# Performance work log

Measured on AMD Instinct MI355X. Metric: run time of the kernel, lower is better.

The kernel has to match this reference:

```python
import jax, jax.numpy as jnp
import numpy as np

BIG = 1e9
EPS_BETA = 1e-6
EPS_BN = 1e-5

N_NODES = 50000
N_EDGES = 800000
IN_DIM = 128
OUT_DIM = 128


def setup_inputs() -> dict:
    key = jax.random.key(0)
    ks = jax.random.split(key, 8)
    h = jax.random.normal(ks[0], (N_NODES, IN_DIM), dtype=jnp.float32)
    src = jax.random.randint(ks[1], (N_EDGES,), 0, N_NODES, dtype=jnp.int32)
    dst = jax.random.randint(ks[2], (N_EDGES,), 0, N_NODES, dtype=jnp.int32)
    sigma_GD = jax.random.uniform(ks[3], (N_EDGES,), dtype=jnp.float32)
    fc_w = jax.random.normal(ks[4], (IN_DIM, OUT_DIM), dtype=jnp.float32) / np.sqrt(IN_DIM)
    fc_b = jax.random.normal(ks[5], (OUT_DIM,), dtype=jnp.float32) * 0.01
    attn_w = jax.random.normal(ks[6], (2 * OUT_DIM, 1), dtype=jnp.float32) / np.sqrt(2 * OUT_DIM)
    attn_b = jax.random.normal(ks[7], (1,), dtype=jnp.float32) * 0.01
    bn_gamma = jnp.ones((OUT_DIM,), dtype=jnp.float32)
    bn_beta = jnp.zeros((OUT_DIM,), dtype=jnp.float32)
    return {"h": h, "src": src, "dst": dst, "sigma_GD": sigma_GD,
            "fc_w": fc_w, "fc_b": fc_b, "attn_w": attn_w, "attn_b": attn_b,
            "bn_gamma": bn_gamma, "bn_beta": bn_beta}


def reference(h, src, dst, sigma_GD, fc_w, fc_b, attn_w, attn_b, bn_gamma, bn_beta):
    n = h.shape[0]
    # node projection
    z = h @ fc_w + fc_b                                   # [N, D]
    z = jnp.where(jnp.isinf(z), BIG, z)
    # per-edge attention logits: concat(src,dst) @ W == src@W1 + dst@W2 (avoid concat materialization)
    d = z.shape[1]
    w_src, w_dst = attn_w[:d], attn_w[d:]
    z_src = z[src]                                        # [E, D]
    a = z_src @ w_src + z[dst] @ w_dst + attn_b           # [E, 1]
    a = jnp.where(jnp.isinf(a), BIG, a)
    e = jax.nn.leaky_relu(a, negative_slope=0.01)[:, 0]   # [E]
    # segment softmax over incoming edges (mailbox softmax)
    m = jax.ops.segment_max(e, dst, num_segments=n)       # [N]
    ex = jnp.exp(e - m[dst])
    denom = jax.ops.segment_sum(ex, dst, num_segments=n)  # [N]
    alpha = ex / denom[dst]                               # [E]
    # beta: sigma_GD normalized per destination node
    bsum = jax.ops.segment_sum(sigma_GD, dst, num_segments=n)
    beta = sigma_GD / (bsum[dst] + EPS_BETA)              # [E]
    # weighted scatter-sum of source features
    h_new = jax.ops.segment_sum((alpha * beta)[:, None] * z_src, dst, num_segments=n)  # [N, D]
    h_new = jnp.where(jnp.isinf(h_new), BIG, h_new)
    # BatchNorm1d (training-mode batch stats, biased variance, as torch does)
    mu = h_new.mean(axis=0)
    var = ((h_new - mu) ** 2).mean(axis=0)
    h_bn = (h_new - mu) * jax.lax.rsqrt(var + EPS_BN) * bn_gamma + bn_beta
    return jax.nn.elu(h_bn)
```

## Files before the change

kernel.cpp:

```cpp
#include <hip/hip_runtime.h>
#include <hip/hip_fp16.h>
#include <math.h>

#define N_NODES 50000
#define N_EDGES 800000
#define BIGV 1000000000.0f
#define NBLK_GEMM 3125
#define CHUNK 1024
#define NCHUNK 782
#define NBUCKET 782
#define NB4 784

typedef _Float16 half8 __attribute__((ext_vector_type(8)));
typedef float floatx4 __attribute__((ext_vector_type(4)));

__device__ __forceinline__ float clampinf(float x) { return isinf(x) ? BIGV : x; }

__device__ __forceinline__ void barrier_lgkm_only() {
    __builtin_amdgcn_sched_barrier(0);
    asm volatile("s_waitcnt lgkmcnt(0)" ::: "memory");
    __builtin_amdgcn_s_barrier();
    __builtin_amdgcn_sched_barrier(0);
}

__global__ __launch_bounds__(256) void k_prep(const float* __restrict__ W,
                                              __half* __restrict__ wt,
                                              float* __restrict__ bns,
                                              const int* __restrict__ dst,
                                              int* __restrict__ countsT)
{
    __shared__ int hist[NB4];
    const int t = threadIdx.x;
    const int idx = blockIdx.x * 256 + t;
    if (idx < 16384) {
        int n = idx >> 7, k = idx & 127;
        wt[idx] = __float2half(W[k * 128 + n]);
    }
    if (idx < 256) bns[idx] = 0.f;
    for (int i = t; i < NB4; i += 256) hist[i] = 0;
    __syncthreads();
    const int base = blockIdx.x * CHUNK;
    for (int i = t; i < CHUNK; i += 256) {
        int e = base + i;
        if (e < N_EDGES) atomicAdd(&hist[dst[e] >> 6], 1);
    }
    __syncthreads();
    for (int i = t; i < NB4; i += 256)
        countsT[i * NB4 + blockIdx.x] = hist[i];
}

__global__ __launch_bounds__(256) void k_off(const int* __restrict__ countsT,
                                             int* __restrict__ cursC,
                                             int* __restrict__ btot)
{
    const int wv = (blockIdx.x << 2) + (threadIdx.x >> 6);
    const int l = threadIdx.x & 63;
    if (wv >= NBUCKET) {
        if (l == 0 && wv < NB4) btot[wv] = 0;
        return;
    }
    const int* row = countsT + (size_t)wv * NB4;
    int carry = 0;
    #pragma unroll
    for (int p = 0; p < 13; ++p) {
        const int c = p * 64 + l;
        const int v = (c < NCHUNK) ? row[c] : 0;
        int x = v;
        #pragma unroll
        for (int o = 1; o < 64; o <<= 1) {
            int u = __shfl_up(x, o);
            if (l >= o) x += u;
        }
        if (c < NCHUNK) cursC[(size_t)c * NB4 + wv] = carry + x - v;
        carry += __shfl(x, 63);
    }
    if (l == 0) btot[wv] = carry;
}

__global__ __launch_bounds__(256) void k_gemm(
    const float* __restrict__ h, const __half* __restrict__ wt,
    const float* __restrict__ bias, const float* __restrict__ attn_w,
    __half* __restrict__ zh, float* __restrict__ sv, float* __restrict__ tv)
{
    __shared__ _Float16 hA[16][136];
    __shared__ float spart[4][16], tpart[4][16];

    const int tid = threadIdx.x;
    const int lane = tid & 63;
    const int wv = tid >> 6;
    const int l16 = lane & 15;
    const int oct = lane >> 4;
    const int n0 = wv << 5;
    const int node0 = blockIdx.x << 4;

    {
        const float4* h4 = (const float4*)(h + (size_t)node0 * 128);
        for (int i = tid; i < 512; i += 256) {
            int r = i >> 5, c4 = i & 31;
            float4 v = h4[i];
            union { __half2 h2[2]; uint2 u; } pk;
            pk.h2[0] = __floats2half2_rn(v.x, v.y);
            pk.h2[1] = __floats2half2_rn(v.z, v.w);
            *(uint2*)&hA[r][c4 << 2] = pk.u;
        }
    }

    half8 bfrag[4][2];
    #pragma unroll
    for (int kk = 0; kk < 4; ++kk)
        #pragma unroll
        for (int t = 0; t < 2; ++t)
            bfrag[kk][t] = *(const half8*)(wt + (size_t)(n0 + t * 16 + l16) * 128
                                              + kk * 32 + oct * 8);

    const float bv0 = bias[n0 + l16],         bv1 = bias[n0 + 16 + l16];
    const float ws0 = attn_w[n0 + l16],       ws1 = attn_w[n0 + 16 + l16];
    const float wd0 = attn_w[128 + n0 + l16], wd1 = attn_w[128 + n0 + 16 + l16];

    barrier_lgkm_only();

    floatx4 acc0 = {0.f, 0.f, 0.f, 0.f};
    floatx4 acc1 = {0.f, 0.f, 0.f, 0.f};
    #pragma unroll
    for (int kk = 0; kk < 4; ++kk) {
        half8 a = *(const half8*)&hA[l16][(kk << 5) + (oct << 3)];
        acc0 = __builtin_amdgcn_mfma_f32_16x16x32_f16(a, bfrag[kk][0], acc0, 0, 0, 0);
        acc1 = __builtin_amdgcn_mfma_f32_16x16x32_f16(a, bfrag[kk][1], acc1, 0, 0, 0);
    }

    float s_acc[4], t_acc[4];
    #pragma unroll
    for (int r = 0; r < 4; ++r) {
        float z0 = clampinf(acc0[r] + bv0);
        float z1 = clampinf(acc1[r] + bv1);
        const int row = (oct << 2) + r;
        zh[(size_t)(node0 + row) * 128 + n0 + l16]      = __float2half(z0);
        zh[(size_t)(node0 + row) * 128 + n0 + 16 + l16] = __float2half(z1);
        s_acc[r] = z0 * ws0 + z1 * ws1;
        t_acc[r] = z0 * wd0 + z1 * wd1;
    }
    #pragma unroll
    for (int r = 0; r < 4; ++r) {
        #pragma unroll
        for (int o = 1; o < 16; o <<= 1) {
            s_acc[r] += __shfl_xor(s_acc[r], o);
            t_acc[r] += __shfl_xor(t_acc[r], o);
        }
    }
    if (l16 == 0) {
        #pragma unroll
        for (int r = 0; r < 4; ++r) {
            spart[wv][(oct << 2) + r] = s_acc[r];
            tpart[wv][(oct << 2) + r] = t_acc[r];
        }
    }
    barrier_lgkm_only();
    if (tid < 16) {
        sv[node0 + tid] = spart[0][tid] + spart[1][tid] + spart[2][tid] + spart[3][tid];
        tv[node0 + tid] = tpart[0][tid] + tpart[1][tid] + tpart[2][tid] + tpart[3][tid];
    }
}

__global__ __launch_bounds__(256) void k_scat(
    const int* __restrict__ src, const int* __restrict__ dst,
    const float* __restrict__ sigma,
    const float* __restrict__ sv, const float* __restrict__ tv,
    const float* __restrict__ attn_b,
    const int* __restrict__ cursC, const int* __restrict__ btot,
    float4* __restrict__ tmp, int* __restrict__ bbase_g)
{
    __shared__ int cur[NB4];
    __shared__ int bb[NB4];
    __shared__ int tsc[256];
    const int t = threadIdx.x;
    const int self = blockIdx.x;

    for (int i = t; i < NB4; i += 256) cur[i] = cursC[(size_t)self * NB4 + i];

    uint4 bt = {0u, 0u, 0u, 0u};
    int tsum = 0;
    if (t < 196) {
        bt = ((const uint4*)btot)[t];
        tsum = (int)(bt.x + bt.y + bt.z + bt.w);
    }
    tsc[t] = tsum;
    __syncthreads();
    for (int off = 1; off < 256; off <<= 1) {
        int u = (t >= off) ? tsc[t - off] : 0;
        __syncthreads();
        tsc[t] += u;
        __syncthreads();
    }
    if (t < 196) {
        const int v0 = tsc[t] - tsum;
        bb[4*t+0] = v0;
        bb[4*t+1] = v0 + (int)bt.x;
        bb[4*t+2] = v0 + (int)bt.x + (int)bt.y;
        bb[4*t+3] = v0 + (int)bt.x + (int)bt.y + (int)bt.z;
    }
    __syncthreads();
    for (int i = t; i < NB4; i += 256) cur[i] += bb[i];
    if (self == 0)
        for (int i = t; i < NB4; i += 256) bbase_g[i] = bb[i];
    __syncthreads();

    const float ab = attn_b[0];
    const int base = self * CHUNK;
    for (int i = t; i < CHUNK; i += 256) {
        int e = base + i;
        if (e < N_EDGES) {
            int s = src[e];
            int d = dst[e];
            float a = sv[s] + tv[d] + ab;
            a = clampinf(a);
            float ev = a > 0.f ? a : 0.01f * a;
            int pos = atomicAdd(&cur[d >> 6], 1);
            float4 rec;
            rec.x = __int_as_float(s);
            rec.y = sigma[e];
            rec.z = ev;
            rec.w = __int_as_float(d);
            tmp[pos] = rec;
        }
    }
}

__global__ __launch_bounds__(256) void k_binB(const float4* __restrict__ tmp,
                                              const int* __restrict__ bbase_g,
                                              int* __restrict__ colptr,
                                              float4* __restrict__ recs)
{
    __shared__ int hist[64];
    __shared__ int cur[64];
    const int t = threadIdx.x;
    const int b = blockIdx.x;
    const int s0 = bbase_g[b];
    const int n = ((b + 1 < NB4) ? bbase_g[b + 1] : N_EDGES) - s0;
    if (t < 64) hist[t] = 0;
    __syncthreads();
    const float* tw = (const float*)tmp;
    for (int i = t; i < n; i += 256) {
        int d = __float_as_int(tw[4 * (size_t)(s0 + i) + 3]);
        atomicAdd(&hist[d & 63], 1);
    }
    __syncthreads();
    if (t < 64) {
        const int hv = hist[t];
        int x = hv;
        #pragma unroll
        for (int o = 1; o < 64; o <<= 1) {
            int u = __shfl_up(x, o);
            if (t >= o) x += u;
        }
        const int excl = x - hv;
        cur[t] = s0 + excl;
        const int node = (b << 6) + t;
        if (node < N_NODES) colptr[node] = s0 + excl;
    }
    if (b == 0 && t == 0) colptr[N_NODES] = N_EDGES;
    __syncthreads();
    for (int i = t; i < n; i += 256) {
        float4 rec = tmp[s0 + i];
        int d = __float_as_int(rec.w);
        int pos = atomicAdd(&cur[d & 63], 1);
        rec.w = 0.f;
        recs[pos] = rec;
    }
}

__global__ __launch_bounds__(256) void k_agg(
    const int* __restrict__ colptr, const float4* __restrict__ recs,
    const __half* __restrict__ zh, float* __restrict__ out)
{
    const int lane = threadIdx.x & 63;
    const int node = blockIdx.x * 4 + (threadIdx.x >> 6);
    if (node >= N_NODES) return;
    const int base = colptr[node];
    const int deg = colptr[node + 1] - base;

    const int grp = lane >> 4;
    const int l16 = lane & 15;
    float acc[8] = {0.f, 0.f, 0.f, 0.f, 0.f, 0.f, 0.f, 0.f};

    if (deg > 0) {
        if (deg <= 64) {
            int sidx = 0; float sig = 0.f, e = -INFINITY;
            if (lane < deg) {
                float4 r = recs[base + lane];
                sidx = __float_as_int(r.x); sig = r.y; e = r.z;
            }
            float m = e;
            for (int o = 32; o; o >>= 1) m = fmaxf(m, __shfl_xor(m, o));
            float p = (lane < deg) ? __expf(e - m) : 0.f;
            float dn = p, bs = sig;
            for (int o = 32; o; o >>= 1) {
                dn += __shfl_xor(dn, o);
                bs += __shfl_xor(bs, o);
            }
            const float coef = p * sig * (1.0f / dn) / (bs + 1e-6f);
            for (int c = 0; c < deg; c += 4) {
                const int j = c + grp;
                const int js = (j < deg) ? j : 0;
                float cf = __shfl(coef, js);
                int sj = __shfl(sidx, js);
                if (j < deg) {
                    uint4 raw = *(const uint4*)(zh + ((size_t)sj << 7) + (l16 << 3));
                    const __half2* hp = (const __half2*)&raw;
                    #pragma unroll
                    for (int k = 0; k < 4; ++k) {
                        float2 f = __half22float2(hp[k]);
                        acc[2*k]   = fmaf(cf, f.x, acc[2*k]);
                        acc[2*k+1] = fmaf(cf, f.y, acc[2*k+1]);
                    }
                }
            }
        } else {
            float m = -INFINITY;
            for (int i = lane; i < deg; i += 64) m = fmaxf(m, recs[base + i].z);
            for (int o = 32; o; o >>= 1) m = fmaxf(m, __shfl_xor(m, o));
            float dn = 0.f, bs = 0.f;
            for (int i = lane; i < deg; i += 64) {
                float4 r = recs[base + i];
                dn += __expf(r.z - m); bs += r.y;
            }
            for (int o = 32; o; o >>= 1) {
                dn += __shfl_xor(dn, o);
                bs += __shfl_xor(bs, o);
            }
            const float scale = (1.0f / dn) / (bs + 1e-6f);
            for (int c = 0; c < deg; c += 64) {
                int i = c + lane;
                int sidx = 0; float coef = 0.f;
                if (i < deg) {
                    float4 r = recs[base + i];
                    sidx = __float_as_int(r.x);
                    coef = __expf(r.z - m) * r.y * scale;
                }
                const int cnt2 = min(64, deg - c);
                for (int j = 0; j < cnt2; j += 4) {
                    const int jj = j + grp;
                    const int js = (jj < cnt2) ? jj : 0;
                    float cf = __shfl(coef, js);
                    int sj = __shfl(sidx, js);
                    if (jj < cnt2) {
                        uint4 raw = *(const uint4*)(zh + ((size_t)sj << 7) + (l16 << 3));
                        const __half2* hp = (const __half2*)&raw;
                        #pragma unroll
                        for (int k = 0; k < 4; ++k) {
                            float2 f = __half22float2(hp[k]);
                            acc[2*k]   = fmaf(cf, f.x, acc[2*k]);
                            acc[2*k+1] = fmaf(cf, f.y, acc[2*k+1]);
                        }
                    }
                }
            }
        }
    }
    #pragma unroll
    for (int k = 0; k < 8; ++k) {
        acc[k] += __shfl_xor(acc[k], 16);
        acc[k] += __shfl_xor(acc[k], 32);
    }
    if (grp == 0) {
        float4 o0, o1;
        o0.x = clampinf(acc[0]); o0.y = clampinf(acc[1]);
        o0.z = clampinf(acc[2]); o0.w = clampinf(acc[3]);
        o1.x = clampinf(acc[4]); o1.y = clampinf(acc[5]);
        o1.z = clampinf(acc[6]); o1.w = clampinf(acc[7]);
        float4* op = (float4*)(out + (size_t)node * 128 + (l16 << 3));
        op[0] = o0; op[1] = o1;
    }
}

__global__ __launch_bounds__(256) void k_bnstats(const float* __restrict__ hnew,
                                                 float* __restrict__ sums)
{
    const int tid = threadIdx.x;
    const int f4 = (tid & 31) << 2;
    const int rgrp = tid >> 5;
    float4 s = {0.f, 0.f, 0.f, 0.f}, q = {0.f, 0.f, 0.f, 0.f};
    for (int node = blockIdx.x * 8 + rgrp; node < N_NODES; node += 256 * 8) {
        float4 v = *(const float4*)(hnew + (size_t)node * 128 + f4);
        s.x += v.x; s.y += v.y; s.z += v.z; s.w += v.w;
        q.x += v.x * v.x; q.y += v.y * v.y; q.z += v.z * v.z; q.w += v.w * v.w;
    }
    __shared__ float4 ls[256], lq[256];
    ls[tid] = s; lq[tid] = q;
    __syncthreads();
    for (int off = 128; off >= 32; off >>= 1) {
        if (tid < off) {
            float4 a = ls[tid + off], b = lq[tid + off];
            ls[tid].x += a.x; ls[tid].y += a.y; ls[tid].z += a.z; ls[tid].w += a.w;
            lq[tid].x += b.x; lq[tid].y += b.y; lq[tid].z += b.z; lq[tid].w += b.w;
        }
        __syncthreads();
    }
    if (tid < 32) {
        float4 fs = ls[tid], fq = lq[tid];
        atomicAdd(&sums[f4 + 0], fs.x);
        atomicAdd(&sums[f4 + 1], fs.y);
        atomicAdd(&sums[f4 + 2], fs.z);
        atomicAdd(&sums[f4 + 3], fs.w);
        atomicAdd(&sums[128 + f4 + 0], fq.x);
        atomicAdd(&sums[128 + f4 + 1], fq.y);
        atomicAdd(&sums[128 + f4 + 2], fq.z);
        atomicAdd(&sums[128 + f4 + 3], fq.w);
    }
}

__global__ __launch_bounds__(256) void k_bnapply(float* __restrict__ io,
                                                 const float* __restrict__ sums,
                                                 const float* __restrict__ gamma,
                                                 const float* __restrict__ beta)
{
    __shared__ float sc[128], sh[128];
    const int tid = threadIdx.x;
    if (tid < 128) {
        const float invn = 1.0f / (float)N_NODES;
        float mu = sums[tid] * invn;
        float var = fmaxf(sums[128 + tid] * invn - mu * mu, 0.f);
        float g = gamma[tid] * rsqrtf(var + 1e-5f);
        sc[tid] = g;
        sh[tid] = beta[tid] - mu * g;
    }
    __syncthreads();
    const size_t idx = (size_t)blockIdx.x * 256 + tid;
    const int f4 = ((int)idx & 31) << 2;
    float4 x = ((const float4*)io)[idx];
    float y0 = x.x * sc[f4 + 0] + sh[f4 + 0];
    float y1 = x.y * sc[f4 + 1] + sh[f4 + 1];
    float y2 = x.z * sc[f4 + 2] + sh[f4 + 2];
    float y3 = x.w * sc[f4 + 3] + sh[f4 + 3];
    float4 o;
    o.x = y0 > 0.f ? y0 : expm1f(y0);
    o.y = y1 > 0.f ? y1 : expm1f(y1);
    o.z = y2 > 0.f ? y2 : expm1f(y2);
    o.w = y3 > 0.f ? y3 : expm1f(y3);
    ((float4*)io)[idx] = o;
}

extern "C" void kernel_launch(void* const* d_in, const int* in_sizes, int n_in,
                              void* d_out, int out_size, void* d_ws, size_t ws_size,
                              hipStream_t stream)
{
    const float* h      = (const float*)d_in[0];
    const int*   src    = (const int*)  d_in[1];
    const int*   dst    = (const int*)  d_in[2];
    const float* sigma  = (const float*)d_in[3];
    const float* fc_w   = (const float*)d_in[4];
    const float* fc_b   = (const float*)d_in[5];
    const float* attn_w = (const float*)d_in[6];
    const float* attn_b = (const float*)d_in[7];
    const float* gamma  = (const float*)d_in[8];
    const float* beta   = (const float*)d_in[9];
    float* out = (float*)d_out;

    float4* recs   = (float4*)d_ws;
    float4* tmp    = recs + N_EDGES;
    __half* zh     = (__half*)(tmp + N_EDGES);
    float*  sv     = (float*)(zh + (size_t)N_NODES * 128);
    float*  tv     = sv + N_NODES;
    float*  bns    = tv + N_NODES;
    int*    colptr = (int*)(bns + 256);
    __half* wt     = (__half*)(colptr + 50004);
    int*    countsT= (int*)(wt + 16384);
    int*    cursC  = countsT + NB4 * NB4;
    int*    btot   = cursC + NB4 * NB4;
    int*    bbase  = btot + NB4;

    k_prep    <<<NCHUNK, 256, 0, stream>>>(fc_w, wt, bns, dst, countsT);
    k_off     <<<196, 256, 0, stream>>>(countsT, cursC, btot);
    k_gemm    <<<NBLK_GEMM, 256, 0, stream>>>(h, wt, fc_b, attn_w, zh, sv, tv);
    k_scat    <<<NCHUNK, 256, 0, stream>>>(src, dst, sigma, sv, tv, attn_b,
                                           cursC, btot, tmp, bbase);
    k_binB    <<<NBUCKET, 256, 0, stream>>>(tmp, bbase, colptr, recs);
    k_agg     <<<N_NODES / 4, 256, 0, stream>>>(colptr, recs, zh, out);
    k_bnstats <<<256, 256, 0, stream>>>(out, bns);
    k_bnapply <<<(N_NODES * 128) / (256 * 4), 256, 0, stream>>>(out, bns, gamma, beta);
}
```

Baseline: 225.4 us.

## Fuse second-level binning with aggregation in LDS; deterministic BN partial reduction

The per-bucket local sort and the per-node aggregation are merged into one kernel. Each bucket's edge records are sorted into shared memory, with a global overflow buffer for buckets larger than the LDS capacity, and each of 8 waves then aggregates its nodes straight from LDS. This removes the global recs/colptr write and reread and one kernel launch, at the cost of fewer, larger blocks (782 blocks of 512 threads) for the gather-heavy aggregation. BN statistics now write per-block partials that a single-block kernel reduces, replacing float atomics and the zero-init.

```diff
diff --git a/kernel.cpp b/kernel.cpp
--- a/kernel.cpp
+++ b/kernel.cpp
@@ -10,6 +10,8 @@
 #define NCHUNK 782
 #define NBUCKET 782
 #define NB4 784
+#define BMAX 1280
+#define NBLK_BN 512
 
 typedef _Float16 half8 __attribute__((ext_vector_type(8)));
 typedef float floatx4 __attribute__((ext_vector_type(4)));
@@ -25,7 +27,6 @@
 
 __global__ __launch_bounds__(256) void k_prep(const float* __restrict__ W,
                                               __half* __restrict__ wt,
-                                              float* __restrict__ bns,
                                               const int* __restrict__ dst,
                                               int* __restrict__ countsT)
 {
@@ -36,7 +37,6 @@
         int n = idx >> 7, k = idx & 127;
         wt[idx] = __float2half(W[k * 128 + n]);
     }
-    if (idx < 256) bns[idx] = 0.f;
     for (int i = t; i < NB4; i += 256) hist[i] = 0;
     __syncthreads();
     const int base = blockIdx.x * CHUNK;
@@ -225,21 +225,24 @@
     }
 }
 
-__global__ __launch_bounds__(256) void k_binB(const float4* __restrict__ tmp,
-                                              const int* __restrict__ bbase_g,
-                                              int* __restrict__ colptr,
-                                              float4* __restrict__ recs)
-{
+__global__ __launch_bounds__(512) void k_bagg(
+    const float4* __restrict__ tmp, const int* __restrict__ bbase_g,
+    const __half* __restrict__ zh, float4* __restrict__ ovf,
+    float* __restrict__ out)
+{
+    __shared__ float4 lrec[BMAX];
     __shared__ int hist[64];
+    __shared__ int segs[65];
     __shared__ int cur[64];
     const int t = threadIdx.x;
     const int b = blockIdx.x;
     const int s0 = bbase_g[b];
-    const int n = ((b + 1 < NB4) ? bbase_g[b + 1] : N_EDGES) - s0;
+    const int n = bbase_g[b + 1] - s0;
+
     if (t < 64) hist[t] = 0;
     __syncthreads();
     const float* tw = (const float*)tmp;
-    for (int i = t; i < n; i += 256) {
+    for (int i = t; i < n; i += 512) {
         int d = __float_as_int(tw[4 * (size_t)(s0 + i) + 3]);
         atomicAdd(&hist[d & 63], 1);
     }
@@ -252,97 +255,55 @@
             int u = __shfl_up(x, o);
             if (t >= o) x += u;
         }
-        const int excl = x - hv;
-        cur[t] = s0 + excl;
-        const int node = (b << 6) + t;
-        if (node < N_NODES) colptr[node] = s0 + excl;
-    }
-    if (b == 0 && t == 0) colptr[N_NODES] = N_EDGES;
-    __syncthreads();
-    for (int i = t; i < n; i += 256) {
+        segs[t] = x - hv;
+        cur[t]  = x - hv;
+        if (t == 63) segs[64] = x;
+    }
+    __syncthreads();
+    for (int i = t; i < n; i += 512) {
         float4 rec = tmp[s0 + i];
         int d = __float_as_int(rec.w);
         int pos = atomicAdd(&cur[d & 63], 1);
-        rec.w = 0.f;
-        recs[pos] = rec;
-    }
-}
-
-__global__ __launch_bounds__(256) void k_agg(
-    const int* __restrict__ colptr, const float4* __restrict__ recs,
-    const __half* __restrict__ zh, float* __restrict__ out)
-{
-    const int lane = threadIdx.x & 63;
-    const int node = blockIdx.x * 4 + (threadIdx.x >> 6);
-    if (node >= N_NODES) return;
-    const int base = colptr[node];
-    const int deg = colptr[node + 1] - base;
-
+        if (pos < BMAX) lrec[pos] = rec;
+        else            ovf[s0 + pos] = rec;
+    }
+    __syncthreads();
+
+    const int lane = t & 63;
+    const int wv = t >> 6;
     const int grp = lane >> 4;
     const int l16 = lane & 15;
-    float acc[8] = {0.f, 0.f, 0.f, 0.f, 0.f, 0.f, 0.f, 0.f};
-
-    if (deg > 0) {
-        if (deg <= 64) {
-            int sidx = 0; float sig = 0.f, e = -INFINITY;
-            if (lane < deg) {
-                float4 r = recs[base + lane];
-                sidx = __float_as_int(r.x); sig = r.y; e = r.z;
-            }
-            float m = e;
-            for (int o = 32; o; o >>= 1) m = fmaxf(m, __shfl_xor(m, o));
-            float p = (lane < deg) ? __expf(e - m) : 0.f;
-            float dn = p, bs = sig;
-            for (int o = 32; o; o >>= 1) {
-                dn += __shfl_xor(dn, o);
-                bs += __shfl_xor(bs, o);
-            }
-            const float coef = p * sig * (1.0f / dn) / (bs + 1e-6f);
-            for (int c = 0; c < deg; c += 4) {
-                const int j = c + grp;
-                const int js = (j < deg) ? j : 0;
-                float cf = __shfl(coef, js);
-                int sj = __shfl(sidx, js);
-                if (j < deg) {
-                    uint4 raw = *(const uint4*)(zh + ((size_t)sj << 7) + (l16 << 3));
-                    const __half2* hp = (const __half2*)&raw;
-                    #pragma unroll
-                    for (int k = 0; k < 4; ++k) {
-                        float2 f = __half22float2(hp[k]);
-                        acc[2*k]   = fmaf(cf, f.x, acc[2*k]);
-                        acc[2*k+1] = fmaf(cf, f.y, acc[2*k+1]);
-                    }
-                }
-            }
-        } else {
-            float m = -INFINITY;
-            for (int i = lane; i < deg; i += 64) m = fmaxf(m, recs[base + i].z);
-            for (int o = 32; o; o >>= 1) m = fmaxf(m, __shfl_xor(m, o));
-            float dn = 0.f, bs = 0.f;
-            for (int i = lane; i < deg; i += 64) {
-                float4 r = recs[base + i];
-                dn += __expf(r.z - m); bs += r.y;
-            }
-            for (int o = 32; o; o >>= 1) {
-                dn += __shfl_xor(dn, o);
-                bs += __shfl_xor(bs, o);
-            }
-            const float scale = (1.0f / dn) / (bs + 1e-6f);
-            for (int c = 0; c < deg; c += 64) {
-                int i = c + lane;
-                int sidx = 0; float coef = 0.f;
-                if (i < deg) {
-                    float4 r = recs[base + i];
-                    sidx = __float_as_int(r.x);
-                    coef = __expf(r.z - m) * r.y * scale;
-                }
-                const int cnt2 = min(64, deg - c);
-                for (int j = 0; j < cnt2; j += 4) {
-                    const int jj = j + grp;
-                    const int js = (jj < cnt2) ? jj : 0;
+
+    for (int j = wv; j < 64; j += 8) {
+        const int node = (b << 6) + j;
+        if (node >= N_NODES) continue;
+        const int beg = segs[j];
+        const int deg = segs[j + 1] - beg;
+        float acc[8] = {0.f, 0.f, 0.f, 0.f, 0.f, 0.f, 0.f, 0.f};
+
+        if (deg > 0) {
+            if (deg <= 64) {
+                int sidx = 0; float sig = 0.f, e = -INFINITY;
+                if (lane < deg) {
+                    const int off = beg + lane;
+                    float4 r = (off < BMAX) ? lrec[off] : ovf[s0 + off];
+                    sidx = __float_as_int(r.x); sig = r.y; e = r.z;
+                }
+                float m = e;
+                for (int o = 32; o; o >>= 1) m = fmaxf(m, __shfl_xor(m, o));
+                float p = (lane < deg) ? __expf(e - m) : 0.f;
+                float dn = p, bs = sig;
+                for (int o = 32; o; o >>= 1) {
+                    dn += __shfl_xor(dn, o);
+                    bs += __shfl_xor(bs, o);
+                }
+                const float coef = p * sig * (1.0f / dn) / (bs + 1e-6f);
+                for (int c = 0; c < deg; c += 4) {
+                    const int jj = c + grp;
+                    const int js = (jj < deg) ? jj : 0;
                     float cf = __shfl(coef, js);
                     int sj = __shfl(sidx, js);
-                    if (jj < cnt2) {
+                    if (jj < deg) {
                         uint4 raw = *(const uint4*)(zh + ((size_t)sj << 7) + (l16 << 3));
                         const __half2* hp = (const __half2*)&raw;
                         #pragma unroll
@@ -353,33 +314,79 @@
                         }
                     }
                 }
+            } else {
+                float m = -INFINITY;
+                for (int i = lane; i < deg; i += 64) {
+                    const int off = beg + i;
+                    float4 r = (off < BMAX) ? lrec[off] : ovf[s0 + off];
+                    m = fmaxf(m, r.z);
+                }
+                for (int o = 32; o; o >>= 1) m = fmaxf(m, __shfl_xor(m, o));
+                float dn = 0.f, bs = 0.f;
+                for (int i = lane; i < deg; i += 64) {
+                    const int off = beg + i;
+                    float4 r = (off < BMAX) ? lrec[off] : ovf[s0 + off];
+                    dn += __expf(r.z - m); bs += r.y;
+                }
+                for (int o = 32; o; o >>= 1) {
+                    dn += __shfl_xor(dn, o);
+                    bs += __shfl_xor(bs, o);
+                }
+                const float scale = (1.0f / dn) / (bs + 1e-6f);
+                for (int c = 0; c < deg; c += 64) {
+                    int i = c + lane;
+                    int sidx = 0; float coef = 0.f;
+                    if (i < deg) {
+                        const int off = beg + i;
+                        float4 r = (off < BMAX) ? lrec[off] : ovf[s0 + off];
+                        sidx = __float_as_int(r.x);
+                        coef = __expf(r.z - m) * r.y * scale;
+                    }
+                    const int cnt2 = min(64, deg - c);
+                    for (int jj = 0; jj < cnt2; jj += 4) {
+                        const int j4 = jj + grp;
+                        const int js = (j4 < cnt2) ? j4 : 0;
+                        float cf = __shfl(coef, js);
+                        int sj = __shfl(sidx, js);
+                        if (j4 < cnt2) {
+                            uint4 raw = *(const uint4*)(zh + ((size_t)sj << 7) + (l16 << 3));
+                            const __half2* hp = (const __half2*)&raw;
+                            #pragma unroll
+                            for (int k = 0; k < 4; ++k) {
+                                float2 f = __half22float2(hp[k]);
+                                acc[2*k]   = fmaf(cf, f.x, acc[2*k]);
+                                acc[2*k+1] = fmaf(cf, f.y, acc[2*k+1]);
+                            }
+                        }
+                    }
+                }
             }
         }
-    }
-    #pragma unroll
-    for (int k = 0; k < 8; ++k) {
-        acc[k] += __shfl_xor(acc[k], 16);
-        acc[k] += __shfl_xor(acc[k], 32);
-    }
-    if (grp == 0) {
-        float4 o0, o1;
-        o0.x = clampinf(acc[0]); o0.y = clampinf(acc[1]);
-        o0.z = clampinf(acc[2]); o0.w = clampinf(acc[3]);
-        o1.x = clampinf(acc[4]); o1.y = clampinf(acc[5]);
-        o1.z = clampinf(acc[6]); o1.w = clampinf(acc[7]);
-        float4* op = (float4*)(out + (size_t)node * 128 + (l16 << 3));
-        op[0] = o0; op[1] = o1;
+        #pragma unroll
+        for (int k = 0; k < 8; ++k) {
+            acc[k] += __shfl_xor(acc[k], 16);
+            acc[k] += __shfl_xor(acc[k], 32);
+        }
+        if (grp == 0) {
+            float4 o0, o1;
+            o0.x = clampinf(acc[0]); o0.y = clampinf(acc[1]);
+            o0.z = clampinf(acc[2]); o0.w = clampinf(acc[3]);
+            o1.x = clampinf(acc[4]); o1.y = clampinf(acc[5]);
+            o1.z = clampinf(acc[6]); o1.w = clampinf(acc[7]);
+            float4* op = (float4*)(out + (size_t)node * 128 + (l16 << 3));
+            op[0] = o0; op[1] = o1;
+        }
     }
 }
 
 __global__ __launch_bounds__(256) void k_bnstats(const float* __restrict__ hnew,
-                                                 float* __restrict__ sums)
+                                                 float* __restrict__ partials)
 {
     const int tid = threadIdx.x;
     const int f4 = (tid & 31) << 2;
     const int rgrp = tid >> 5;
     float4 s = {0.f, 0.f, 0.f, 0.f}, q = {0.f, 0.f, 0.f, 0.f};
-    for (int node = blockIdx.x * 8 + rgrp; node < N_NODES; node += 256 * 8) {
+    for (int node = blockIdx.x * 8 + rgrp; node < N_NODES; node += NBLK_BN * 8) {
         float4 v = *(const float4*)(hnew + (size_t)node * 128 + f4);
         s.x += v.x; s.y += v.y; s.z += v.z; s.w += v.w;
         q.x += v.x * v.x; q.y += v.y * v.y; q.z += v.z * v.z; q.w += v.w * v.w;
@@ -396,16 +403,27 @@
         __syncthreads();
     }
     if (tid < 32) {
-        float4 fs = ls[tid], fq = lq[tid];
-        atomicAdd(&sums[f4 + 0], fs.x);
-        atomicAdd(&sums[f4 + 1], fs.y);
-        atomicAdd(&sums[f4 + 2], fs.z);
-        atomicAdd(&sums[f4 + 3], fs.w);
-        atomicAdd(&sums[128 + f4 + 0], fq.x);
-        atomicAdd(&sums[128 + f4 + 1], fq.y);
-        atomicAdd(&sums[128 + f4 + 2], fq.z);
-        atomicAdd(&sums[128 + f4 + 3], fq.w);
-    }
+        float* p = partials + (size_t)blockIdx.x * 256;
+        *(float4*)(p + f4)       = ls[tid];
+        *(float4*)(p + 128 + f4) = lq[tid];
+    }
+}
+
+__global__ __launch_bounds__(1024) void k_bnred(const float* __restrict__ partials,
+                                                float* __restrict__ sums)
+{
+    __shared__ float red[4][256];
+    const int t = threadIdx.x;
+    const int f = t & 255;
+    const int part = t >> 8;
+    float s = 0.f;
+    #pragma unroll 8
+    for (int b = part * (NBLK_BN / 4); b < (part + 1) * (NBLK_BN / 4); ++b)
+        s += partials[(size_t)b * 256 + f];
+    red[part][f] = s;
+    __syncthreads();
+    if (part == 0)
+        sums[f] = red[0][f] + red[1][f] + red[2][f] + red[3][f];
 }
 
 __global__ __launch_bounds__(256) void k_bnapply(float* __restrict__ io,
@@ -455,26 +473,26 @@
     const float* beta   = (const float*)d_in[9];
     float* out = (float*)d_out;
 
-    float4* recs   = (float4*)d_ws;
-    float4* tmp    = recs + N_EDGES;
-    __half* zh     = (__half*)(tmp + N_EDGES);
+    float4* tmp    = (float4*)d_ws;
+    float4* ovf    = tmp + N_EDGES;
+    __half* zh     = (__half*)(ovf + N_EDGES);
     float*  sv     = (float*)(zh + (size_t)N_NODES * 128);
     float*  tv     = sv + N_NODES;
     float*  bns    = tv + N_NODES;
-    int*    colptr = (int*)(bns + 256);
-    __half* wt     = (__half*)(colptr + 50004);
+    float*  parts  = bns + 256;
+    __half* wt     = (__half*)(parts + NBLK_BN * 256);
     int*    countsT= (int*)(wt + 16384);
     int*    cursC  = countsT + NB4 * NB4;
     int*    btot   = cursC + NB4 * NB4;
     int*    bbase  = btot + NB4;
 
-    k_prep    <<<NCHUNK, 256, 0, stream>>>(fc_w, wt, bns, dst, countsT);
+    k_prep    <<<NCHUNK, 256, 0, stream>>>(fc_w, wt, dst, countsT);
     k_off     <<<196, 256, 0, stream>>>(countsT, cursC, btot);
     k_gemm    <<<NBLK_GEMM, 256, 0, stream>>>(h, wt, fc_b, attn_w, zh, sv, tv);
     k_scat    <<<NCHUNK, 256, 0, stream>>>(src, dst, sigma, sv, tv, attn_b,
                                            cursC, btot, tmp, bbase);
-    k_binB    <<<NBUCKET, 256, 0, stream>>>(tmp, bbase, colptr, recs);
-    k_agg     <<<N_NODES / 4, 256, 0, stream>>>(colptr, recs, zh, out);
-    k_bnstats <<<256, 256, 0, stream>>>(out, bns);
+    k_bagg    <<<NBUCKET, 512, 0, stream>>>(tmp, bbase, zh, ovf, out);
+    k_bnstats <<<NBLK_BN, 256, 0, stream>>>(out, parts);
+    k_bnred   <<<1, 1024, 0, stream>>>(parts, bns);
     k_bnapply <<<(N_NODES * 128) / (256 * 4), 256, 0, stream>>>(out, bns, gamma, beta);
 }
```

Measured after the change: 210.3 us. 1.07x faster.
